# Kernel tuning notes

Measured on AMD Instinct MI355X. Metric: run time of the kernel, lower is better.

The kernel has to match this reference:

```python
import jax, jax.numpy as jnp
import numpy as np

T, B, IN, H, OUT = 2048, 64, 128, 256, 128


def setup_inputs() -> dict:
    key = jax.random.key(0)
    ks = jax.random.split(key, 7)
    s_ih = 1.0 / np.sqrt(H)
    return {
        "input": jax.random.normal(ks[0], (T, B, IN), dtype=jnp.float32),
        "W_ih": jax.random.uniform(ks[1], (4 * H, IN), minval=-s_ih, maxval=s_ih, dtype=jnp.float32),
        "W_hh": jax.random.uniform(ks[2], (4 * H, H), minval=-s_ih, maxval=s_ih, dtype=jnp.float32),
        "b_ih": jax.random.uniform(ks[3], (4 * H,), minval=-s_ih, maxval=s_ih, dtype=jnp.float32),
        "b_hh": jax.random.uniform(ks[4], (4 * H,), minval=-s_ih, maxval=s_ih, dtype=jnp.float32),
        "W_out": jax.random.uniform(ks[5], (OUT, H), minval=-s_ih, maxval=s_ih, dtype=jnp.float32),
        "b_out": jax.random.uniform(ks[6], (OUT,), minval=-s_ih, maxval=s_ih, dtype=jnp.float32),
    }


def reference(input, W_ih, W_hh, b_ih, b_hh, W_out, b_out):
    # input: [T, B, IN]. PyTorch LSTMCell gate order: i, f, g, o (chunks of H).
    H_ = W_hh.shape[1]
    # Precompute input-side gate pre-activations for all timesteps: [T, B, 4H]
    x_gates = jnp.einsum("tbi,gi->tbg", input, W_ih) + b_ih + b_hh

    def step(carry, xg):
        h, c = carry
        gates = xg + h @ W_hh.T  # [B, 4H]
        i = jax.nn.sigmoid(gates[:, 0 * H_:1 * H_])
        f = jax.nn.sigmoid(gates[:, 1 * H_:2 * H_])
        g = jnp.tanh(gates[:, 2 * H_:3 * H_])
        o = jax.nn.sigmoid(gates[:, 3 * H_:4 * H_])
        c_new = f * c + i * g
        h_new = o * jnp.tanh(c_new)
        y = h_new @ W_out.T + b_out  # [B, OUT]
        return (h_new, c_new), y

    Bsz = input.shape[1]
    h0 = jnp.zeros((Bsz, H_), dtype=input.dtype)
    c0 = jnp.zeros((Bsz, H_), dtype=input.dtype)
    (h_T, c_T), outputs = jax.lax.scan(step, (h0, c0), x_gates)
    return outputs, (h_T, c_T)
```

## Files before the change

### kernel.cpp

```cpp
#include <hip/hip_runtime.h>
#include <cstdint>
#include <cstddef>

#define TT   2048
#define BB   64
#define IND  128
#define HH   256
#define GG   1024
#define OUTD 128
#define TC   64
#define NCH  (TT / TC)

static const size_t XG0_OFF    = 0;
static const size_t XG1_OFF    = 8388608ull;
static const size_t HST0_OFF   = 16777216ull;
static const size_t HST1_OFF   = 18874368ull;
static const size_t WHH_OFF    = 20971520ull;
static const size_t WIH_OFF    = WHH_OFF  + 524288ull;
static const size_t WOUT_OFF   = WIH_OFF  + 262144ull;
static const size_t BSUM_OFF   = WOUT_OFF + 65536ull;
static const size_t HSTATE_OFF = BSUM_OFF + 4096ull;
static const size_t CSTATE_OFF = HSTATE_OFF + 32768ull;
static const size_t WS_NEEDED  = CSTATE_OFF + 65536ull;

static const int SMEM_SZ = 65536 + 512 + 4096;

typedef _Float16 h2 __attribute__((ext_vector_type(2)));

union U16 { uint4 u; h2 h[4]; };
union HU  { unsigned short u; _Float16 h; };

__device__ __forceinline__ float fdot2f(h2 a, h2 b, float c) {
#if __has_builtin(__builtin_amdgcn_fdot2)
  return __builtin_amdgcn_fdot2(a, b, c, false);
#else
  return c + (float)a.x * (float)b.x + (float)a.y * (float)b.y;
#endif
}

__device__ __forceinline__ float sigm(float x) { return 1.f / (1.f + __expf(-x)); }
__device__ __forceinline__ float tanh_fast(float x) {
  float ax = fabsf(x);
  float e  = __expf(-2.f * ax);
  float r  = (1.f - e) / (1.f + e);
  return x < 0.f ? -r : r;
}

__global__ void k0_pack(const float* __restrict__ Whh, const float* __restrict__ Wih,
                        const float* __restrict__ Wout, const float* __restrict__ bih,
                        const float* __restrict__ bhh, uint8_t* __restrict__ ws) {
  int tid = blockIdx.x * 256 + threadIdx.x;
  if (tid < 32768) {
    int rr = tid >> 13, rem = tid & 8191;
    int hf = rem >> 12, q = (rem >> 8) & 15, u = rem & 255;
    int row = (rr == 0) ? u : (rr == 1) ? 256 + u : (rr == 2) ? 768 + u : 512 + u;
    int kb = hf * 128 + q * 8;
    const float4* s = (const float4*)(Whh + (size_t)row * HH + kb);
    float4 v0 = s[0], v1 = s[1];
    U16 o;
    o.h[0].x = (_Float16)v0.x; o.h[0].y = (_Float16)v0.y;
    o.h[1].x = (_Float16)v0.z; o.h[1].y = (_Float16)v0.w;
    o.h[2].x = (_Float16)v1.x; o.h[2].y = (_Float16)v1.y;
    o.h[3].x = (_Float16)v1.z; o.h[3].y = (_Float16)v1.w;
    ((uint4*)(ws + WHH_OFF))[tid] = o.u;
  } else if (tid < 65536) {
    int t2 = tid - 32768;
    ((_Float16*)(ws + WOUT_OFF))[t2] = (_Float16)Wout[t2];
  } else if (tid < 81920) {
    int i = tid - 65536;
    const float4* s = (const float4*)(Wih + (size_t)i * 8);
    float4 v0 = s[0], v1 = s[1];
    U16 o;
    o.h[0].x = (_Float16)v0.x; o.h[0].y = (_Float16)v0.y;
    o.h[1].x = (_Float16)v0.z; o.h[1].y = (_Float16)v0.w;
    o.h[2].x = (_Float16)v1.x; o.h[2].y = (_Float16)v1.y;
    o.h[3].x = (_Float16)v1.z; o.h[3].y = (_Float16)v1.w;
    ((uint4*)(ws + WIH_OFF))[i] = o.u;
  } else if (tid < 82944) {
    int n = tid - 81920;
    ((float*)(ws + BSUM_OFF))[n] = bih[n] + bhh[n];
  }
}

__global__ void __launch_bounds__(256) k1_xgemm(const float* __restrict__ x,
                                                uint8_t* __restrict__ ws) {
  const uint4* Wp   = (const uint4*)(ws + WIH_OFF);
  const float* bsum = (const float*)(ws + BSUM_OFF);
  _Float16*    xg   = (_Float16*)(ws + XG0_OFF);

  const int s = blockIdx.x >> 4;
  const int m = ((blockIdx.x & 15) << 8) + threadIdx.x;

  __shared__ uint4 wlds[1024];
  __shared__ float bsl[64];
  #pragma unroll
  for (int i = 0; i < 4; ++i)
    wlds[i * 256 + threadIdx.x] = Wp[(size_t)(s << 6) * 16 + i * 256 + threadIdx.x];
  if (threadIdx.x < 64) bsl[threadIdx.x] = bsum[(s << 6) + threadIdx.x];
  __syncthreads();

  const float4* xr = (const float4*)(x + (size_t)m * IND);
  h2 xv[64];
  #pragma unroll
  for (int i = 0; i < 32; ++i) {
    float4 v = xr[i];
    xv[2*i  ].x = (_Float16)v.x; xv[2*i  ].y = (_Float16)v.y;
    xv[2*i+1].x = (_Float16)v.z; xv[2*i+1].y = (_Float16)v.w;
  }
  _Float16* xgrow = xg + (size_t)m * GG + (s << 6);
  for (int g = 0; g < 8; ++g) {
    float acc[8];
    #pragma unroll
    for (int j = 0; j < 8; ++j) {
      const uint4* wr = &wlds[(g * 8 + j) * 16];
      float a = bsl[g * 8 + j];
      #pragma unroll
      for (int q = 0; q < 16; ++q) {
        U16 w; w.u = wr[q];
        a = fdot2f(w.h[0], xv[4*q+0], a);
        a = fdot2f(w.h[1], xv[4*q+1], a);
        a = fdot2f(w.h[2], xv[4*q+2], a);
        a = fdot2f(w.h[3], xv[4*q+3], a);
      }
      acc[j] = a;
    }
    U16 o;
    #pragma unroll
    for (int p = 0; p < 4; ++p) { o.h[p].x = (_Float16)acc[2*p]; o.h[p].y = (_Float16)acc[2*p+1]; }
    *(uint4*)(xgrow + g * 8) = o.u;
  }
}

__global__ void __launch_bounds__(512, 2) k2_fused(const float* __restrict__ x,
                                                   uint8_t* __restrict__ ws,
                                                   const float* __restrict__ b_out,
                                                   float* __restrict__ out, int ch) {
  extern __shared__ __align__(16) uint8_t smem[];
  const int bi  = blockIdx.x;
  const int tid = threadIdx.x;

  if (bi < 64) {
    if (ch >= NCH) return;
    const int b    = bi;
    const int u    = tid & 255;
    const int half = tid >> 8;
    const int t0   = ch * TC;

    const uint4* WR = (const uint4*)(ws + WHH_OFF);
    const uint4* WG = WR + 24576;
    const unsigned short* xp = (const unsigned short*)(ws + ((ch & 1) ? XG1_OFF : XG0_OFF));
    _Float16* hst    = (_Float16*)(ws + ((ch & 1) ? HST1_OFF : HST0_OFF));
    _Float16* hstate = (_Float16*)(ws + HSTATE_OFF);
    float*    cstate = (float*)(ws + CSTATE_OFF);

    uint4*    gws   = (uint4*)smem;
    _Float16* h_lds = (_Float16*)(smem + 65536);
    float*    ps_i  = (float*)(smem + 65536 + 512);
    float*    ps_f  = ps_i + 256;
    float*    ps_g  = ps_f + 256;
    float*    ps_o  = ps_g + 256;

    h2 wi[64], wf[64], wo[64];
    #pragma unroll
    for (int q = 0; q < 16; ++q) {
      U16 a;
      a.u = WR[(size_t)((0 * 2 + half) * 16 + q) * 256 + u];
      wi[4*q+0]=a.h[0]; wi[4*q+1]=a.h[1]; wi[4*q+2]=a.h[2]; wi[4*q+3]=a.h[3];
      a.u = WR[(size_t)((1 * 2 + half) * 16 + q) * 256 + u];
      wf[4*q+0]=a.h[0]; wf[4*q+1]=a.h[1]; wf[4*q+2]=a.h[2]; wf[4*q+3]=a.h[3];
      a.u = WR[(size_t)((2 * 2 + half) * 16 + q) * 256 + u];
      wo[4*q+0]=a.h[0]; wo[4*q+1]=a.h[1]; wo[4*q+2]=a.h[2]; wo[4*q+3]=a.h[3];
    }
    #pragma unroll
    for (int j = 0; j < 8; ++j) {
      int idx = j * 512 + tid;
      int hf = idx >> 11, q2 = (idx >> 8) & 7, u2 = idx & 255;
      gws[idx] = WG[(size_t)(hf * 16 + q2) * 256 + u2];
    }
    const uint4* gl  = gws + half * 2048 + u;
    const uint4* wgp = WG + (size_t)(half * 16) * 256 + u;

    if (tid < 32) {
      uint4 z = make_uint4(0u, 0u, 0u, 0u);
      ((uint4*)h_lds)[tid] = (t0 == 0) ? z : ((const uint4*)(hstate + (size_t)b * HH))[tid];
    }
    float c = 0.f;
    if (half == 0 && t0 != 0) c = cstate[(size_t)b * HH + u];

    const size_t xrow = (size_t)b * GG;
    HU xi, xf, xgv, xo;
    if (half == 0) {
      xi.u  = xp[xrow + u];
      xf.u  = xp[xrow + 256 + u];
      xgv.u = xp[xrow + 512 + u];
      xo.u  = xp[xrow + 768 + u];
    }
    __syncthreads();

    for (int tt = 0; tt < TC; ++tt) {
      float ai = 0.f, af = 0.f, ag = 0.f, ao = 0.f;
      const uint4* hv = ((const uint4*)h_lds) + half * 16;
      #pragma unroll
      for (int q = 0; q < 8; ++q) {
        U16 hh;  hh.u  = hv[q];
        U16 wg_; wg_.u = gl[q * 256];
        #pragma unroll
        for (int j = 0; j < 4; ++j) {
          ai = fdot2f(wi[4*q+j], hh.h[j], ai);
          af = fdot2f(wf[4*q+j], hh.h[j], af);
          ag = fdot2f(wg_.h[j],  hh.h[j], ag);
          ao = fdot2f(wo[4*q+j], hh.h[j], ao);
        }
      }
      #pragma unroll
      for (int q = 8; q < 16; ++q) {
        U16 hh;  hh.u  = hv[q];
        U16 wg_; wg_.u = wgp[(size_t)q * 256];
        #pragma unroll
        for (int j = 0; j < 4; ++j) {
          ai = fdot2f(wi[4*q+j], hh.h[j], ai);
          af = fdot2f(wf[4*q+j], hh.h[j], af);
          ag = fdot2f(wg_.h[j],  hh.h[j], ag);
          ao = fdot2f(wo[4*q+j], hh.h[j], ao);
        }
      }
      if (half == 1) { ps_i[u] = ai; ps_f[u] = af; ps_g[u] = ag; ps_o[u] = ao; }
      __syncthreads();
      if (half == 0) {
        float gi = sigm(ai + ps_i[u] + (float)xi.h);
        float gf = sigm(af + ps_f[u] + (float)xf.h);
        float gg = tanh_fast(ag + ps_g[u] + (float)xgv.h);
        float go = sigm(ao + ps_o[u] + (float)xo.h);
        c = gf * c + gi * gg;
        float hn = go * tanh_fast(c);
        h_lds[u] = (_Float16)hn;
        hst[((size_t)tt * BB + b) * HH + u] = (_Float16)hn;
        if (tt + 1 < TC) {
          const size_t nx = xrow + (size_t)(tt + 1) * (BB * GG);
          xi.u  = xp[nx + u];
          xf.u  = xp[nx + 256 + u];
          xgv.u = xp[nx + 512 + u];
          xo.u  = xp[nx + 768 + u];
        }
        if (t0 + tt == TT - 1) {
          const size_t tail = (size_t)TT * BB * OUTD;
          out[tail + (size_t)b * HH + u] = hn;
          out[tail + (size_t)BB * HH + (size_t)b * HH + u] = c;
        }
      }
      __syncthreads();
    }

    if (tid < 32) ((uint4*)(hstate + (size_t)b * HH))[tid] = ((const uint4*)h_lds)[tid];
    if (half == 0) cstate[(size_t)b * HH + u] = c;

  } else if (bi < 192) {
    if (ch + 1 >= NCH) return;
    const int p    = bi - 64;
    const int seg  = p >> 3;
    const int rowg = p & 7;
    const int m    = rowg * 512 + tid;
    const int t0n  = (ch + 1) * TC;

    const uint4* Wp   = (const uint4*)(ws + WIH_OFF);
    const float* bsum = (const float*)(ws + BSUM_OFF);
    _Float16*    xgn  = (_Float16*)(ws + (((ch + 1) & 1) ? XG1_OFF : XG0_OFF));

    uint4* wlds = (uint4*)smem;
    float* bsl  = (float*)(smem + 16384);
    wlds[tid]       = Wp[(size_t)(seg << 6) * 16 + tid];
    wlds[tid + 512] = Wp[(size_t)(seg << 6) * 16 + 512 + tid];
    if (tid < 64) bsl[tid] = bsum[(seg << 6) + tid];
    __syncthreads();

    const float4* xr = (const float4*)(x + ((size_t)t0n * BB + m) * IND);
    h2 xv[64];
    #pragma unroll
    for (int i = 0; i < 32; ++i) {
      float4 v = xr[i];
      xv[2*i  ].x = (_Float16)v.x; xv[2*i  ].y = (_Float16)v.y;
      xv[2*i+1].x = (_Float16)v.z; xv[2*i+1].y = (_Float16)v.w;
    }
    _Float16* xgrow = xgn + (size_t)m * GG + (seg << 6);
    for (int g = 0; g < 8; ++g) {
      float acc[8];
      #pragma unroll
      for (int j = 0; j < 8; ++j) {
        const uint4* wr = &wlds[(g * 8 + j) * 16];
        float a = bsl[g * 8 + j];
        #pragma unroll
        for (int q = 0; q < 16; ++q) {
          U16 w; w.u = wr[q];
          a = fdot2f(w.h[0], xv[4*q+0], a);
          a = fdot2f(w.h[1], xv[4*q+1], a);
          a = fdot2f(w.h[2], xv[4*q+2], a);
          a = fdot2f(w.h[3], xv[4*q+3], a);
        }
        acc[j] = a;
      }
      U16 o;
      #pragma unroll
      for (int pk = 0; pk < 4; ++pk) { o.h[pk].x = (_Float16)acc[2*pk]; o.h[pk].y = (_Float16)acc[2*pk+1]; }
      *(uint4*)(xgrow + g * 8) = o.u;
    }

  } else {
    if (ch < 1) return;
    const int yb   = bi - 192;
    const int seg  = yb & 15;
    const int rowg = yb >> 4;
    const int t0p  = (ch - 1) * TC;

    const _Float16* hstp = (const _Float16*)(ws + (((ch - 1) & 1) ? HST1_OFF : HST0_OFF));
    const uint4* WO = (const uint4*)(ws + WOUT_OFF);

    uint4* wlds = (uint4*)smem;
    float* bsl  = (float*)(smem + 4096);
    if (tid < 256) wlds[tid] = WO[(size_t)(seg * 8) * 32 + tid];
    if (tid < 8)   bsl[tid]  = b_out[seg * 8 + tid];
    __syncthreads();

    #pragma unroll
    for (int rr = 0; rr < 4; ++rr) {
      const int r = rowg * 2048 + rr * 512 + tid;
      const uint4* hr = (const uint4*)(hstp + (size_t)r * HH);
      float acc[8];
      #pragma unroll
      for (int j = 0; j < 8; ++j) acc[j] = bsl[j];
      #pragma unroll 4
      for (int q = 0; q < 32; ++q) {
        U16 hh; hh.u = hr[q];
        #pragma unroll
        for (int j = 0; j < 8; ++j) {
          U16 w; w.u = wlds[j * 32 + q];
          acc[j] = fdot2f(w.h[0], hh.h[0], acc[j]);
          acc[j] = fdot2f(w.h[1], hh.h[1], acc[j]);
          acc[j] = fdot2f(w.h[2], hh.h[2], acc[j]);
          acc[j] = fdot2f(w.h[3], hh.h[3], acc[j]);
        }
      }
      float* orow = out + ((size_t)t0p * BB + r) * OUTD + seg * 8;
      *(float4*)(orow)     = make_float4(acc[0], acc[1], acc[2], acc[3]);
      *(float4*)(orow + 4) = make_float4(acc[4], acc[5], acc[6], acc[7]);
    }
  }
}

extern "C" void kernel_launch(void* const* d_in, const int* in_sizes, int n_in,
                              void* d_out, int out_size, void* d_ws, size_t ws_size,
                              hipStream_t stream) {
  const float* input = (const float*)d_in[0];
  const float* W_ih  = (const float*)d_in[1];
  const float* W_hh  = (const float*)d_in[2];
  const float* b_ih  = (const float*)d_in[3];
  const float* b_hh  = (const float*)d_in[4];
  const float* W_out = (const float*)d_in[5];
  const float* b_out = (const float*)d_in[6];
  float*   out = (float*)d_out;
  uint8_t* ws  = (uint8_t*)d_ws;

  if (ws_size < WS_NEEDED) return;

  hipFuncSetAttribute((const void*)k2_fused,
                      hipFuncAttributeMaxDynamicSharedMemorySize, SMEM_SZ);

  hipLaunchKernelGGL(k0_pack,  dim3(324), dim3(256), 0, stream,
                     W_hh, W_ih, W_out, b_ih, b_hh, ws);
  hipLaunchKernelGGL(k1_xgemm, dim3(256), dim3(256), 0, stream, input, ws);
  for (int ch = 0; ch <= NCH; ++ch) {
    hipLaunchKernelGGL(k2_fused, dim3(224), dim3(512), SMEM_SZ, stream,
                       input, ws, b_out, out, ch);
  }
}
```

Measured before the change: 4.375 ms.

## Interleave K-halves across lane pairs, reduce via shuffle, double-buffer h in LDS

The recurrent kernel now assigns the two K-halves of each hidden unit to adjacent lanes and combines the partial sums with a lane shuffle, replacing the LDS partial-sum exchange and one of the two block barriers per timestep. The h vector is double-buffered in LDS so the next step's writes do not race with current reads. The whole g-gate weight slice (128 KB) now sits in shared memory instead of half in LDS and half streamed from global, and the W_hh pack layout is reordered to match. Both lanes of a pair now compute the activations redundantly, and the larger LDS footprint may lower occupancy, which matters for the co-scheduled producer blocks in the same launch.

New measurement: 3.720 ms. 1.18x faster.

```diff
diff --git a/kernel.cpp b/kernel.cpp
--- a/kernel.cpp
+++ b/kernel.cpp
@@ -23,7 +23,7 @@
 static const size_t CSTATE_OFF = HSTATE_OFF + 32768ull;
 static const size_t WS_NEEDED  = CSTATE_OFF + 65536ull;
 
-static const int SMEM_SZ = 65536 + 512 + 4096;
+static const int SMEM_SZ = 131072 + 1024;
 
 typedef _Float16 h2 __attribute__((ext_vector_type(2)));
 
@@ -52,7 +52,8 @@
   int tid = blockIdx.x * 256 + threadIdx.x;
   if (tid < 32768) {
     int rr = tid >> 13, rem = tid & 8191;
-    int hf = rem >> 12, q = (rem >> 8) & 15, u = rem & 255;
+    int q = rem >> 9, u2 = rem & 511;
+    int u = u2 >> 1, hf = u2 & 1;
     int row = (rr == 0) ? u : (rr == 1) ? 256 + u : (rr == 2) ? 768 + u : 512 + u;
     int kb = hf * 128 + q * 8;
     const float4* s = (const float4*)(Whh + (size_t)row * HH + kb);
@@ -142,8 +143,8 @@
   if (bi < 64) {
     if (ch >= NCH) return;
     const int b    = bi;
-    const int u    = tid & 255;
-    const int half = tid >> 8;
+    const int u    = tid >> 1;
+    const int half = tid & 1;
     const int t0   = ch * TC;
 
     const uint4* WR = (const uint4*)(ws + WHH_OFF);
@@ -154,56 +155,44 @@
     float*    cstate = (float*)(ws + CSTATE_OFF);
 
     uint4*    gws   = (uint4*)smem;
-    _Float16* h_lds = (_Float16*)(smem + 65536);
-    float*    ps_i  = (float*)(smem + 65536 + 512);
-    float*    ps_f  = ps_i + 256;
-    float*    ps_g  = ps_f + 256;
-    float*    ps_o  = ps_g + 256;
+    _Float16* h_lds = (_Float16*)(smem + 131072);
 
     h2 wi[64], wf[64], wo[64];
     #pragma unroll
     for (int q = 0; q < 16; ++q) {
       U16 a;
-      a.u = WR[(size_t)((0 * 2 + half) * 16 + q) * 256 + u];
+      a.u = WR[q * 512 + tid];
       wi[4*q+0]=a.h[0]; wi[4*q+1]=a.h[1]; wi[4*q+2]=a.h[2]; wi[4*q+3]=a.h[3];
-      a.u = WR[(size_t)((1 * 2 + half) * 16 + q) * 256 + u];
+      a.u = WR[8192 + q * 512 + tid];
       wf[4*q+0]=a.h[0]; wf[4*q+1]=a.h[1]; wf[4*q+2]=a.h[2]; wf[4*q+3]=a.h[3];
-      a.u = WR[(size_t)((2 * 2 + half) * 16 + q) * 256 + u];
+      a.u = WR[16384 + q * 512 + tid];
       wo[4*q+0]=a.h[0]; wo[4*q+1]=a.h[1]; wo[4*q+2]=a.h[2]; wo[4*q+3]=a.h[3];
     }
     #pragma unroll
-    for (int j = 0; j < 8; ++j) {
-      int idx = j * 512 + tid;
-      int hf = idx >> 11, q2 = (idx >> 8) & 7, u2 = idx & 255;
-      gws[idx] = WG[(size_t)(hf * 16 + q2) * 256 + u2];
-    }
-    const uint4* gl  = gws + half * 2048 + u;
-    const uint4* wgp = WG + (size_t)(half * 16) * 256 + u;
+    for (int j = 0; j < 16; ++j) gws[j * 512 + tid] = WG[j * 512 + tid];
 
     if (tid < 32) {
       uint4 z = make_uint4(0u, 0u, 0u, 0u);
       ((uint4*)h_lds)[tid] = (t0 == 0) ? z : ((const uint4*)(hstate + (size_t)b * HH))[tid];
     }
     float c = 0.f;
-    if (half == 0 && t0 != 0) c = cstate[(size_t)b * HH + u];
+    if (t0 != 0) c = cstate[(size_t)b * HH + u];
 
     const size_t xrow = (size_t)b * GG;
     HU xi, xf, xgv, xo;
-    if (half == 0) {
-      xi.u  = xp[xrow + u];
-      xf.u  = xp[xrow + 256 + u];
-      xgv.u = xp[xrow + 512 + u];
-      xo.u  = xp[xrow + 768 + u];
-    }
+    xi.u  = xp[xrow + u];
+    xf.u  = xp[xrow + 256 + u];
+    xgv.u = xp[xrow + 512 + u];
+    xo.u  = xp[xrow + 768 + u];
     __syncthreads();
 
     for (int tt = 0; tt < TC; ++tt) {
       float ai = 0.f, af = 0.f, ag = 0.f, ao = 0.f;
-      const uint4* hv = ((const uint4*)h_lds) + half * 16;
-      #pragma unroll
-      for (int q = 0; q < 8; ++q) {
+      const uint4* hv = ((const uint4*)h_lds) + (tt & 1) * 32 + half * 16;
+      #pragma unroll
+      for (int q = 0; q < 16; ++q) {
         U16 hh;  hh.u  = hv[q];
-        U16 wg_; wg_.u = gl[q * 256];
+        U16 wg_; wg_.u = gws[q * 512 + tid];
         #pragma unroll
         for (int j = 0; j < 4; ++j) {
           ai = fdot2f(wi[4*q+j], hh.h[j], ai);
@@ -212,41 +201,31 @@
           ao = fdot2f(wo[4*q+j], hh.h[j], ao);
         }
       }
-      #pragma unroll
-      for (int q = 8; q < 16; ++q) {
-        U16 hh;  hh.u  = hv[q];
-        U16 wg_; wg_.u = wgp[(size_t)q * 256];
-        #pragma unroll
-        for (int j = 0; j < 4; ++j) {
-          ai = fdot2f(wi[4*q+j], hh.h[j], ai);
-          af = fdot2f(wf[4*q+j], hh.h[j], af);
-          ag = fdot2f(wg_.h[j],  hh.h[j], ag);
-          ao = fdot2f(wo[4*q+j], hh.h[j], ao);
-        }
-      }
-      if (half == 1) { ps_i[u] = ai; ps_f[u] = af; ps_g[u] = ag; ps_o[u] = ao; }
-      __syncthreads();
+      ai += __shfl_xor(ai, 1);
+      af += __shfl_xor(af, 1);
+      ag += __shfl_xor(ag, 1);
+      ao += __shfl_xor(ao, 1);
+      float gi = sigm(ai + (float)xi.h);
+      float gf = sigm(af + (float)xf.h);
+      float gg = tanh_fast(ag + (float)xgv.h);
+      float go = sigm(ao + (float)xo.h);
+      c = gf * c + gi * gg;
+      float hn = go * tanh_fast(c);
       if (half == 0) {
-        float gi = sigm(ai + ps_i[u] + (float)xi.h);
-        float gf = sigm(af + ps_f[u] + (float)xf.h);
-        float gg = tanh_fast(ag + ps_g[u] + (float)xgv.h);
-        float go = sigm(ao + ps_o[u] + (float)xo.h);
-        c = gf * c + gi * gg;
-        float hn = go * tanh_fast(c);
-        h_lds[u] = (_Float16)hn;
+        h_lds[((tt + 1) & 1) * HH + u] = (_Float16)hn;
         hst[((size_t)tt * BB + b) * HH + u] = (_Float16)hn;
-        if (tt + 1 < TC) {
-          const size_t nx = xrow + (size_t)(tt + 1) * (BB * GG);
-          xi.u  = xp[nx + u];
-          xf.u  = xp[nx + 256 + u];
-          xgv.u = xp[nx + 512 + u];
-          xo.u  = xp[nx + 768 + u];
-        }
         if (t0 + tt == TT - 1) {
           const size_t tail = (size_t)TT * BB * OUTD;
           out[tail + (size_t)b * HH + u] = hn;
           out[tail + (size_t)BB * HH + (size_t)b * HH + u] = c;
         }
+      }
+      if (tt + 1 < TC) {
+        const size_t nx = xrow + (size_t)(tt + 1) * (BB * GG);
+        xi.u  = xp[nx + u];
+        xf.u  = xp[nx + 256 + u];
+        xgv.u = xp[nx + 512 + u];
+        xo.u  = xp[nx + 768 + u];
       }
       __syncthreads();
     }
```
